# Optimization experiments

Measured on AMD Instinct MI355X. Metric: run time of the kernel, lower is better.

## Reference

```python
import jax, jax.numpy as jnp
import numpy as np

B, N, D, H, NCB, TOPK = 4, 2048, 256, 2048, 256, 16
DP = D // 4
SCALE = float(np.sqrt(DP))
THRESH = 0.7
EPS = 1e-8


def setup_inputs() -> dict:
    key = jax.random.key(0)
    ks = jax.random.split(key, 12)
    g = lambda i, shape, s=1.0: jax.random.normal(ks[i], shape, jnp.float32) * s
    return {
        "agent_states": g(0, (B, N, D)),
        "agent_actions": g(1, (B, N, D)),
        "episodic_mem": g(2, (B, N, H)),
        "Wq": g(3, (D, DP), 0.05), "bq": jnp.zeros((DP,), jnp.float32),
        "Wk": g(4, (D, DP), 0.05), "bk": jnp.zeros((DP,), jnp.float32),
        "log_temp": jnp.asarray(0.0, jnp.float32),
        "Wc": g(5, (D, DP), 0.05), "bc": jnp.zeros((DP,), jnp.float32),
        "temp_coal": jnp.asarray(10.0, jnp.float32),
        "W_to_hdc": g(6, (D, H), 0.05), "b_to_hdc": jnp.zeros((H,), jnp.float32),
        "W_from_hdc": g(7, (H, D), 0.02), "b_from_hdc": jnp.zeros((D,), jnp.float32),
        "agent_keys": jnp.sign(g(8, (N, H))),
        "position_codes": jnp.sign(g(9, (NCB, H))),
        "step": 3,
    }


def _cosine(a, b):
    # torch F.cosine_similarity semantics, dim=-1, eps=1e-8
    na = jnp.maximum(jnp.linalg.norm(a, axis=-1), EPS)
    nb = jnp.maximum(jnp.linalg.norm(b, axis=-1), EPS)
    return jnp.sum(a * b, axis=-1) / (na * nb)


def _to_hdc_ste(x):
    soft = jnp.tanh(x * 3.0)
    hard = jnp.sign(x)
    hard = jnp.where(hard == 0, jnp.ones_like(hard), hard)
    return soft + jax.lax.stop_gradient(hard - soft)


def reference(agent_states, agent_actions, episodic_mem, Wq, bq, Wk, bk,
              log_temp, Wc, bc, temp_coal, W_to_hdc, b_to_hdc,
              W_from_hdc, b_from_hdc, agent_keys, position_codes, step):
    # ---- DynamicGraph.compute_graph: top-k dynamic attention adjacency ----
    Q = agent_actions @ Wq + bq                      # (B,N,DP)
    K = agent_actions @ Wk + bk                      # (B,N,DP)
    temp = jnp.clip(jnp.exp(log_temp), 0.1, 10.0)
    scores = jnp.einsum('bnd,bmd->bnm', Q, K) / (SCALE * temp)   # (B,N,N)
    _, topk_idx = jax.lax.top_k(scores, TOPK)                     # (B,N,k)
    bI = jnp.arange(B)[:, None, None]
    nI = jnp.arange(N)[None, :, None]
    mask = jnp.zeros_like(scores).at[bI, nI, topk_idx].set(1.0)   # scatter, like torch scatter_
    scores = scores * mask + (1.0 - mask) * -1e9
    adjacency = jax.nn.softmax(scores, axis=-1)
    # message passing over dynamic graph
    incoming = jnp.einsum('bnm,bmd->bnd', adjacency, agent_states)

    # ---- AgentCombination: sigmoid-normalized coalition mixing ----
    proj = agent_actions @ Wc + bc                   # (B,N,DP)
    pn = proj / jnp.maximum(jnp.linalg.norm(proj, axis=-1, keepdims=True), 1e-12)
    sim = jnp.einsum('bnd,bmd->bnm', pn, pn)
    cw = jax.nn.sigmoid((sim - THRESH) * temp_coal)
    cw = cw / (jnp.sum(cw, axis=-1, keepdims=True) + EPS)
    combined = jnp.einsum('bnm,bmd->bnd', cw, incoming)
    mixed = 0.8 * incoming + 0.2 * combined          # (B,N,D)

    # ---- HDCMemory: bind / write / read with STE ----
    q = _to_hdc_ste(mixed @ W_to_hdc + b_to_hdc)     # (B,N,H) bipolar via STE
    pq = q * agent_keys[None]                        # bind with agent key
    mem = jax.lax.stop_gradient(episodic_mem)        # memory read is detached in original
    pos_code = position_codes[step % NCB]            # (H,)
    new_mem = 0.95 * mem + 0.05 * (q * pos_code)     # write: bind + decay bundle
    strength = jax.nn.sigmoid(_cosine(new_mem, pq))[..., None]   # read similarity
    recall = (new_mem @ W_from_hdc + b_from_hdc) * strength      # (B,N,D)
    return mixed + recall
```

## Files before the change

kernel.cpp:

```cpp
#include <hip/hip_runtime.h>
#include <math.h>

#define BATCH 4
#define NN 2048
#define DD 256
#define HH 2048
#define DP 64
#define KTOP 16

typedef float f32x4 __attribute__((ext_vector_type(4)));
typedef short short8 __attribute__((ext_vector_type(8)));
typedef short short4v __attribute__((ext_vector_type(4)));

__device__ __forceinline__ short f2bf(float x) {
    union { float f; unsigned u; } v; v.f = x;
    unsigned r = v.u + 0x7FFFu + ((v.u >> 16) & 1u);
    return (short)(r >> 16);
}
__device__ __forceinline__ float bf2f(short s) {
    union { unsigned u; float f; } v; v.u = ((unsigned)(unsigned short)s) << 16;
    return v.f;
}

__global__ __launch_bounds__(256) void head_kernel(
    const float* __restrict__ act,
    const float* __restrict__ Wq, const float* __restrict__ bq,
    const float* __restrict__ Wk, const float* __restrict__ bk,
    const float* __restrict__ Wc, const float* __restrict__ bc,
    const float* __restrict__ W2h, const float* __restrict__ Wfh,
    float* __restrict__ Qo, float* __restrict__ Ko, short* __restrict__ Pno,
    short* __restrict__ W2hT_hi, short* __restrict__ W2hT_lo,
    short* __restrict__ WfhT_hi, short* __restrict__ WfhT_lo)
{
    __shared__ float smem[16 * 256];

    if (blockIdx.x < 512) {
        float (*rowbuf)[256] = (float(*)[256])smem;
        const int row0 = blockIdx.x * 16;
        const int t = threadIdx.x;
        const int wave = t >> 6, lane = t & 63;
        const float* src = act + (size_t)row0 * DD;
        for (int i = t; i < 16 * DD; i += 256) rowbuf[i >> 8][i & 255] = src[i];
        __syncthreads();

        float q[4], k[4], c[4];
        #pragma unroll
        for (int r = 0; r < 4; ++r) { q[r] = bq[lane]; k[r] = bk[lane]; c[r] = bc[lane]; }

        for (int d = 0; d < DD; ++d) {
            float wq = Wq[d * DP + lane];
            float wk = Wk[d * DP + lane];
            float wc = Wc[d * DP + lane];
            #pragma unroll
            for (int r = 0; r < 4; ++r) {
                float av = rowbuf[wave * 4 + r][d];
                q[r] = fmaf(av, wq, q[r]);
                k[r] = fmaf(av, wk, k[r]);
                c[r] = fmaf(av, wc, c[r]);
            }
        }
        #pragma unroll
        for (int r = 0; r < 4; ++r) {
            float ss = c[r] * c[r];
            #pragma unroll
            for (int off = 32; off; off >>= 1) ss += __shfl_xor(ss, off);
            float nrm = fmaxf(sqrtf(ss), 1e-12f);
            size_t o = (size_t)(row0 + wave * 4 + r) * DP + lane;
            Qo[o] = q[r];
            Ko[o] = k[r];
            Pno[o] = f2bf(c[r] / nrm);
        }
    } else {
        float (*tile)[33] = (float(*)[33])smem;
        int b = blockIdx.x - 512;
        const float* src; short *dhi, *dlo; int R, C, r0, c0;
        if (b < 512) {
            src = W2h; dhi = W2hT_hi; dlo = W2hT_lo; R = 256; C = 2048;
            r0 = (b >> 6) * 32; c0 = (b & 63) * 32;
        } else {
            b -= 512;
            src = Wfh; dhi = WfhT_hi; dlo = WfhT_lo; R = 2048; C = 256;
            r0 = (b >> 3) * 32; c0 = (b & 7) * 32;
        }
        int tx = threadIdx.x & 31, ty = threadIdx.x >> 5;
        #pragma unroll
        for (int i = 0; i < 4; ++i)
            tile[ty + 8 * i][tx] = src[(size_t)(r0 + ty + 8 * i) * C + c0 + tx];
        __syncthreads();
        #pragma unroll
        for (int i = 0; i < 4; ++i) {
            float v = tile[tx][ty + 8 * i];
            short hi = f2bf(v);
            size_t o = (size_t)(c0 + ty + 8 * i) * R + r0 + tx;
            dhi[o] = hi;
            dlo[o] = f2bf(v - bf2f(hi));
        }
    }
}

__global__ __launch_bounds__(512, 4) void attn_fused_kernel(
    const float* __restrict__ Q, const float* __restrict__ K,
    const float* __restrict__ log_temp,
    const float* __restrict__ states, float* __restrict__ incoming)
{
    const int t = threadIdx.x;
    const int w = t >> 6, l = t & 63;
    const int row = blockIdx.x * 8 + w;
    const int b = row >> 11;

    __shared__ float Ksh[128][68];

    const float temp = fminf(fmaxf(expf(log_temp[0]), 0.1f), 10.0f);
    const float scale = 1.0f / (8.0f * temp);

    const float* Kb = K + (size_t)b * NN * DP;
    const float4* qr4 = (const float4*)(Q + (size_t)row * DP);

    float sc[32];

    for (int ch = 0; ch < 16; ++ch) {
        __syncthreads();
        {
            int r = t >> 2, seg = t & 3;
            const float4* src = (const float4*)(Kb + (size_t)(ch * 128 + r) * DP + seg * 16);
            float4* dst = (float4*)&Ksh[r][seg * 16];
            dst[0] = src[0]; dst[1] = src[1]; dst[2] = src[2]; dst[3] = src[3];
        }
        __syncthreads();
        float a0 = 0.f, a1 = 0.f;
        const float4* k0 = (const float4*)&Ksh[l][0];
        const float4* k1 = (const float4*)&Ksh[64 + l][0];
        #pragma unroll
        for (int h = 0; h < 2; ++h) {
            float4 q[8];
            #pragma unroll
            for (int i = 0; i < 8; ++i) q[i] = qr4[h * 8 + i];
            #pragma unroll
            for (int i = 0; i < 8; ++i) {
                float4 kv0 = k0[h * 8 + i];
                float4 kv1 = k1[h * 8 + i];
                a0 = fmaf(kv0.x, q[i].x, fmaf(kv0.y, q[i].y, fmaf(kv0.z, q[i].z, fmaf(kv0.w, q[i].w, a0))));
                a1 = fmaf(kv1.x, q[i].x, fmaf(kv1.y, q[i].y, fmaf(kv1.z, q[i].z, fmaf(kv1.w, q[i].w, a1))));
            }
        }
        sc[ch * 2]     = a0 * scale;
        sc[ch * 2 + 1] = a1 * scale;
    }

    float wv = 0.f; int wm = 0;
    for (int it = 0; it < KTOP; ++it) {
        float bv = sc[0]; int bs = 0;
        #pragma unroll
        for (int i = 1; i < 32; ++i) {
            bool g = sc[i] > bv;
            bv = g ? sc[i] : bv;
            bs = g ? i : bs;
        }
        int bm = (bs >> 1) * 128 + (bs & 1) * 64 + l;
        #pragma unroll
        for (int off = 1; off < 64; off <<= 1) {
            float ov = __shfl_xor(bv, off);
            int   om = __shfl_xor(bm, off);
            bool take = (ov > bv) || (ov == bv && om < bm);
            bv = take ? ov : bv;
            bm = take ? om : bm;
        }
        if (l == it) { wv = bv; wm = bm; }
        if ((bm & 63) == l) {
            int s = ((bm >> 7) << 1) | ((bm >> 6) & 1);
            #pragma unroll
            for (int i = 0; i < 32; ++i) if (s == i) sc[i] = -3.0e38f;
        }
    }

    float mx = __shfl(wv, 0);
    float e = (l < KTOP) ? expf(wv - mx) : 0.f;
    float Z = e;
    #pragma unroll
    for (int off = 1; off < 64; off <<= 1) Z += __shfl_xor(Z, off);
    float wnorm = e / Z;

    const float* Sb = states + (size_t)b * NN * DD;
    f32x4 acc = (f32x4){0.f, 0.f, 0.f, 0.f};
    #pragma unroll
    for (int kk = 0; kk < KTOP; ++kk) {
        float wk = __shfl(wnorm, kk);
        int   ik = __shfl(wm, kk);
        const float4 v = *(const float4*)(Sb + (size_t)ik * DD + l * 4);
        acc[0] = fmaf(wk, v.x, acc[0]);
        acc[1] = fmaf(wk, v.y, acc[1]);
        acc[2] = fmaf(wk, v.z, acc[2]);
        acc[3] = fmaf(wk, v.w, acc[3]);
    }
    *(float4*)(incoming + (size_t)row * DD + l * 4) = *(float4*)&acc;
}

__global__ __launch_bounds__(256) void coal_kernel(
    const short* __restrict__ pnb_g, const float* __restrict__ incoming,
    const float* __restrict__ temp_coal, float* __restrict__ mixed)
{
    const int b  = blockIdx.x >> 7;
    const int rem = blockIdx.x & 127;
    const int n0 = (rem >> 1) * 32;
    const int dh = rem & 1;
    const int t = threadIdx.x;
    const int w = t >> 6;
    const int l = t & 63;

    __shared__ alignas(16) short pnA[32][72];
    __shared__ alignas(16) short pnB[64][72];
    __shared__ alignas(16) short cwt[32][72];
    __shared__ alignas(16) short incT[128][72];
    __shared__ float rowsum[32];

    const size_t bbase = (size_t)b * NN;

    {
        int r = t >> 3, k8 = (t & 7) * 8;
        *(short8*)&pnA[r][k8] = *(const short8*)(pnb_g + (bbase + n0 + r) * DP + k8);
    }
    if (t < 32) rowsum[t] = 0.0f;

    const float tc = temp_coal[0];

    f32x4 acc[2][2];
    #pragma unroll
    for (int i = 0; i < 2; ++i)
        #pragma unroll
        for (int j = 0; j < 2; ++j)
            acc[i][j] = (f32x4){0.f, 0.f, 0.f, 0.f};

    const int lrow = l & 15;
    const int lk   = (l >> 4) * 8;

    for (int ch = 0; ch < 32; ++ch) {
        const int m0 = ch * 64;
        __syncthreads();

        {
            int r = t >> 2, kq = (t & 3) * 16;
            const short* src = pnb_g + (bbase + m0 + r) * DP + kq;
            *(short8*)&pnB[r][kq]     = *(const short8*)src;
            *(short8*)&pnB[r][kq + 8] = *(const short8*)(src + 8);
        }
        {
            int d4 = t & 31;
            int mg = t >> 5;
            const float* incb = incoming + (bbase + m0) * DD + dh * 128 + d4 * 4;
            #pragma unroll
            for (int i = 0; i < 8; ++i) {
                int m = mg * 8 + i;
                float4 v = *(const float4*)(incb + (size_t)m * DD);
                int db = d4 * 4;
                incT[db + 0][m] = f2bf(v.x);
                incT[db + 1][m] = f2bf(v.y);
                incT[db + 2][m] = f2bf(v.z);
                incT[db + 3][m] = f2bf(v.w);
            }
        }
        __syncthreads();

        f32x4 sacc[2];
        sacc[0] = (f32x4){0.f, 0.f, 0.f, 0.f};
        sacc[1] = (f32x4){0.f, 0.f, 0.f, 0.f};
        #pragma unroll
        for (int ks = 0; ks < 2; ++ks) {
            short8 bfr = *(const short8*)&pnB[w * 16 + lrow][lk + ks * 32];
            short8 a0  = *(const short8*)&pnA[lrow][lk + ks * 32];
            short8 a1  = *(const short8*)&pnA[16 + lrow][lk + ks * 32];
            sacc[0] = __builtin_amdgcn_mfma_f32_16x16x32_bf16(a0, bfr, sacc[0], 0, 0, 0);
            sacc[1] = __builtin_amdgcn_mfma_f32_16x16x32_bf16(a1, bfr, sacc[1], 0, 0, 0);
        }
        #pragma unroll
        for (int rt = 0; rt < 2; ++rt) {
            #pragma unroll
            for (int j = 0; j < 4; ++j) {
                int rr = rt * 16 + (l >> 4) * 4 + j;
                int cc = w * 16 + lrow;
                float cv = 1.0f / (1.0f + expf(-(sacc[rt][j] - 0.7f) * tc));
                cwt[rr][cc] = f2bf(cv);
            }
        }
        __syncthreads();

        {
            int r = t >> 3, c8 = (t & 7) * 8;
            short8 cv = *(const short8*)&cwt[r][c8];
            float p = 0.f;
            #pragma unroll
            for (int j = 0; j < 8; ++j) p += bf2f(cv[j]);
            p += __shfl_xor(p, 1);
            p += __shfl_xor(p, 2);
            p += __shfl_xor(p, 4);
            if ((t & 7) == 0) rowsum[r] += p;
        }

        #pragma unroll
        for (int ks = 0; ks < 2; ++ks) {
            short8 a0 = *(const short8*)&cwt[lrow][lk + ks * 32];
            short8 a1 = *(const short8*)&cwt[16 + lrow][lk + ks * 32];
            #pragma unroll
            for (int ct = 0; ct < 2; ++ct) {
                short8 bfr = *(const short8*)&incT[w * 32 + ct * 16 + lrow][lk + ks * 32];
                acc[0][ct] = __builtin_amdgcn_mfma_f32_16x16x32_bf16(a0, bfr, acc[0][ct], 0, 0, 0);
                acc[1][ct] = __builtin_amdgcn_mfma_f32_16x16x32_bf16(a1, bfr, acc[1][ct], 0, 0, 0);
            }
        }
    }
    __syncthreads();

    #pragma unroll
    for (int rt = 0; rt < 2; ++rt) {
        #pragma unroll
        for (int ct = 0; ct < 2; ++ct) {
            #pragma unroll
            for (int j = 0; j < 4; ++j) {
                int rr = rt * 16 + (l >> 4) * 4 + j;
                int cc = w * 32 + ct * 16 + lrow;
                float inv = 1.0f / (rowsum[rr] + 1e-8f);
                float comb = acc[rt][ct][j] * inv;
                size_t gi = (bbase + n0 + rr) * DD + dh * 128 + cc;
                mixed[gi] = 0.8f * incoming[gi] + 0.2f * comb;
            }
        }
    }
}

__global__ __launch_bounds__(256) void hdcA_kernel(
    const float* __restrict__ mixed,
    const short* __restrict__ W2hT_hi, const short* __restrict__ W2hT_lo,
    const float* __restrict__ b2h,
    unsigned short* __restrict__ qbits)
{
    const int rb = blockIdx.x >> 3;
    const int hs = blockIdx.x & 7;
    const int row0 = rb * 32;
    const int hbase = hs * 256;
    const int t = threadIdx.x;
    const int w = t >> 6, l = t & 63;
    const int lr = l & 15, lg = l >> 4;

    __shared__ short Ahi[32][264], Alo[32][264];
    __shared__ short Whi[64][136], Wlo[64][136];

    #pragma unroll
    for (int i = 0; i < 8; ++i) {
        int idx = t + i * 256;
        int r = idx >> 6, c = (idx & 63) * 4;
        float4 v = *(const float4*)(mixed + (size_t)(row0 + r) * DD + c);
        short4v hi4, lo4;
        hi4[0] = f2bf(v.x); lo4[0] = f2bf(v.x - bf2f(hi4[0]));
        hi4[1] = f2bf(v.y); lo4[1] = f2bf(v.y - bf2f(hi4[1]));
        hi4[2] = f2bf(v.z); lo4[2] = f2bf(v.z - bf2f(hi4[2]));
        hi4[3] = f2bf(v.w); lo4[3] = f2bf(v.w - bf2f(hi4[3]));
        *(short4v*)&Ahi[r][c] = hi4;
        *(short4v*)&Alo[r][c] = lo4;
    }

    for (int ch = 0; ch < 4; ++ch) {
        const int h0 = hbase + ch * 64;
        f32x4 zac[2];
        zac[0] = (f32x4){0.f, 0.f, 0.f, 0.f};
        zac[1] = (f32x4){0.f, 0.f, 0.f, 0.f};
        #pragma unroll
        for (int ks = 0; ks < 2; ++ks) {
            const int k0 = ks * 128;
            __syncthreads();
            {
                int r = t >> 2, cb = (t & 3) * 32;
                const short* sh = W2hT_hi + (size_t)(h0 + r) * DD + k0 + cb;
                const short* sl = W2hT_lo + (size_t)(h0 + r) * DD + k0 + cb;
                #pragma unroll
                for (int j = 0; j < 4; ++j) {
                    *(short8*)&Whi[r][cb + j * 8] = *(const short8*)(sh + j * 8);
                    *(short8*)&Wlo[r][cb + j * 8] = *(const short8*)(sl + j * 8);
                }
            }
            __syncthreads();
            #pragma unroll
            for (int kt = 0; kt < 4; ++kt) {
                int kk = k0 + kt * 32 + lg * 8;
                int kw = kt * 32 + lg * 8;
                short8 bhi = *(const short8*)&Whi[w * 16 + lr][kw];
                short8 blo = *(const short8*)&Wlo[w * 16 + lr][kw];
                #pragma unroll
                for (int mt = 0; mt < 2; ++mt) {
                    short8 ahi = *(const short8*)&Ahi[mt * 16 + lr][kk];
                    short8 alo = *(const short8*)&Alo[mt * 16 + lr][kk];
                    zac[mt] = __builtin_amdgcn_mfma_f32_16x16x32_bf16(ahi, bhi, zac[mt], 0, 0, 0);
                    zac[mt] = __builtin_amdgcn_mfma_f32_16x16x32_bf16(ahi, blo, zac[mt], 0, 0, 0);
                    zac[mt] = __builtin_amdgcn_mfma_f32_16x16x32_bf16(alo, bhi, zac[mt], 0, 0, 0);
                }
            }
        }
        const float bv = b2h[h0 + w * 16 + lr];
        #pragma unroll
        for (int mt = 0; mt < 2; ++mt) {
            #pragma unroll
            for (int j = 0; j < 4; ++j) {
                float z = zac[mt][j] + bv;
                unsigned long long bal = __ballot(z >= 0.0f);
                if (lr == 0)
                    qbits[(size_t)(row0 + mt * 16 + lg * 4 + j) * 128 + (h0 >> 4) + w] =
                        (unsigned short)((bal >> (lg * 16)) & 0xFFFFull);
            }
        }
    }
}

__global__ __launch_bounds__(512) void hdcB_kernel(
    const float* __restrict__ mem, const unsigned short* __restrict__ qbits,
    const float* __restrict__ pos_codes, const int* __restrict__ step,
    const short* __restrict__ WfhT_hi,
    const float* __restrict__ bfh, const float* __restrict__ keys,
    const float* __restrict__ mixed, float* __restrict__ out)
{
    const int mb = blockIdx.x >> 1, nb = blockIdx.x & 1;
    const int row0 = mb * 32, d0 = nb * 128;
    const int t = threadIdx.x;
    const int w = t >> 6, l = t & 63;
    const int wm = w >> 2, wn = w & 3;
    const int lr = l & 15, lg = l >> 4;

    __shared__ short Ahi[32][72], Alo[32][72];
    __shared__ short Bhi[128][72];
    __shared__ float sred[32][2];
    __shared__ float strenL[32];

    int st = ((step[0] % 256) + 256) % 256;
    const float* pos = pos_codes + (size_t)st * HH;

    f32x4 acc[2];
    acc[0] = (f32x4){0.f, 0.f, 0.f, 0.f};
    acc[1] = (f32x4){0.f, 0.f, 0.f, 0.f};
    float pnum = 0.f, pns = 0.f;

    const int ar = t >> 4;
    const int ah = (t & 15) * 4;
    const int arow = row0 + ar;
    const size_t memb = (size_t)arow * HH;
    const size_t keyb = (size_t)(arow & (NN - 1)) * HH;

    for (int kc = 0; kc < 32; ++kc) {
        const int h0 = kc * 64;
        __syncthreads();
        {
            float4 mv = *(const float4*)(mem + memb + h0 + ah);
            float4 kv = *(const float4*)(keys + keyb + h0 + ah);
            float4 pv = *(const float4*)(pos + h0 + ah);
            unsigned bits = (unsigned)qbits[(size_t)arow * 128 + ((h0 + ah) >> 4)] >> (ah & 15);
            float mvs[4] = { mv.x, mv.y, mv.z, mv.w };
            float kvs[4] = { kv.x, kv.y, kv.z, kv.w };
            float pvs[4] = { pv.x, pv.y, pv.z, pv.w };
            short4v hi4, lo4;
            #pragma unroll
            for (int j = 0; j < 4; ++j) {
                float q = ((bits >> j) & 1u) ? 1.0f : -1.0f;
                float nmv = fmaf(0.05f * q, pvs[j], 0.95f * mvs[j]);
                pnum = fmaf(nmv, q * kvs[j], pnum);
                pns  = fmaf(nmv, nmv, pns);
                hi4[j] = f2bf(nmv);
                lo4[j] = f2bf(nmv - bf2f(hi4[j]));
            }
            *(short4v*)&Ahi[ar][ah] = hi4;
            *(short4v*)&Alo[ar][ah] = lo4;
        }
        {
            int r = t >> 2, hb = (t & 3) * 16;
            const short* sh = WfhT_hi + (size_t)(d0 + r) * HH + h0 + hb;
            *(short8*)&Bhi[r][hb]     = *(const short8*)sh;
            *(short8*)&Bhi[r][hb + 8] = *(const short8*)(sh + 8);
        }
        __syncthreads();
        #pragma unroll
        for (int kt = 0; kt < 2; ++kt) {
            const int kk = kt * 32 + lg * 8;
            short8 ahi = *(const short8*)&Ahi[wm * 16 + lr][kk];
            short8 alo = *(const short8*)&Alo[wm * 16 + lr][kk];
            #pragma unroll
            for (int nt = 0; nt < 2; ++nt) {
                short8 bhi = *(const short8*)&Bhi[wn * 32 + nt * 16 + lr][kk];
                acc[nt] = __builtin_amdgcn_mfma_f32_16x16x32_bf16(ahi, bhi, acc[nt], 0, 0, 0);
                acc[nt] = __builtin_amdgcn_mfma_f32_16x16x32_bf16(alo, bhi, acc[nt], 0, 0, 0);
            }
        }
    }

    #pragma unroll
    for (int off = 1; off < 16; off <<= 1) {
        pnum += __shfl_xor(pnum, off);
        pns  += __shfl_xor(pns, off);
    }
    if ((t & 15) == 0) { sred[ar][0] = pnum; sred[ar][1] = pns; }
    __syncthreads();
    if (t < 32) {
        float cosv = sred[t][0] / (fmaxf(sqrtf(sred[t][1]), 1e-8f) * sqrtf(2048.0f));
        strenL[t] = 1.0f / (1.0f + expf(-cosv));
    }
    __syncthreads();

    #pragma unroll
    for (int nt = 0; nt < 2; ++nt) {
        #pragma unroll
        for (int j = 0; j < 4; ++j) {
            int rloc = wm * 16 + lg * 4 + j;
            int col = d0 + wn * 32 + nt * 16 + lr;
            size_t gi = (size_t)(row0 + rloc) * DD + col;
            out[gi] = mixed[gi] + (acc[nt][j] + bfh[col]) * strenL[rloc];
        }
    }
}

extern "C" void kernel_launch(void* const* d_in, const int* in_sizes, int n_in,
                              void* d_out, int out_size, void* d_ws, size_t ws_size,
                              hipStream_t stream) {
    const float* states    = (const float*)d_in[0];
    const float* actions   = (const float*)d_in[1];
    const float* mem       = (const float*)d_in[2];
    const float* Wq        = (const float*)d_in[3];
    const float* bq        = (const float*)d_in[4];
    const float* Wk        = (const float*)d_in[5];
    const float* bk        = (const float*)d_in[6];
    const float* log_temp  = (const float*)d_in[7];
    const float* Wc        = (const float*)d_in[8];
    const float* bc        = (const float*)d_in[9];
    const float* temp_coal = (const float*)d_in[10];
    const float* W2h       = (const float*)d_in[11];
    const float* b2h       = (const float*)d_in[12];
    const float* Wfh       = (const float*)d_in[13];
    const float* bfh       = (const float*)d_in[14];
    const float* keys      = (const float*)d_in[15];
    const float* pos_codes = (const float*)d_in[16];
    const int*   step      = (const int*)d_in[17];
    float* out = (float*)d_out;

    float* ws = (float*)d_ws;
    float* mixed    = ws;
    short* W2hT_hi  = (short*)(mixed + 2097152);
    short* W2hT_lo  = W2hT_hi + 524288;
    short* WfhT_hi  = W2hT_lo + 524288;
    short* WfhT_lo  = WfhT_hi + 524288;
    unsigned short* qbits = (unsigned short*)(WfhT_lo + 524288);
    float* Q        = (float*)(qbits + 1048576);
    float* K        = Q + 524288;
    float* incoming = K + 524288;
    short* pn_bf    = (short*)(incoming + 2097152);

    head_kernel<<<1536, 256, 0, stream>>>(actions, Wq, bq, Wk, bk, Wc, bc, W2h, Wfh,
                                          Q, K, pn_bf, W2hT_hi, W2hT_lo, WfhT_hi, WfhT_lo);
    attn_fused_kernel<<<BATCH * NN / 8, 512, 0, stream>>>(Q, K, log_temp, states, incoming);
    coal_kernel<<<BATCH * (NN / 32) * 2, 256, 0, stream>>>(pn_bf, incoming, temp_coal, mixed);
    hdcA_kernel<<<(BATCH * NN / 32) * 8, 256, 0, stream>>>(mixed, W2hT_hi, W2hT_lo, b2h, qbits);
    hdcB_kernel<<<(BATCH * NN / 32) * 2, 512, 0, stream>>>(mem, qbits, pos_codes, step,
                                                           WfhT_hi, bfh, keys, mixed, out);
}
```

Baseline: 336.4 us.

## Compute attention scores with split-bf16 MFMA instead of scalar FP32 FMAs

The head kernel now splits Q and K into three bf16 parts (hi, mid, lo), and the attention kernel computes QK^T scores with six bf16 MFMA products that approximate FP32 accuracy. The scores go into a shared-memory buffer, and each wave then reads back its row for the existing top-k selection. This replaces the scalar FMA loop and its staging of K tiles in LDS. It adds extra MFMA work and Q/K traffic, uses a 64KB shared buffer that limits occupancy, and small rounding differences could change top-k ties. The qbits buffer now aliases Qh, which is reused after the attention kernel finishes.

New measurement: 356.2 us. +5.9%, slower.

```diff
diff --git a/kernel.cpp b/kernel.cpp
--- a/kernel.cpp
+++ b/kernel.cpp
@@ -28,7 +28,9 @@
     const float* __restrict__ Wk, const float* __restrict__ bk,
     const float* __restrict__ Wc, const float* __restrict__ bc,
     const float* __restrict__ W2h, const float* __restrict__ Wfh,
-    float* __restrict__ Qo, float* __restrict__ Ko, short* __restrict__ Pno,
+    short* __restrict__ Qh, short* __restrict__ Qm, short* __restrict__ Ql,
+    short* __restrict__ Kh, short* __restrict__ Km, short* __restrict__ Kl,
+    short* __restrict__ Pno,
     short* __restrict__ W2hT_hi, short* __restrict__ W2hT_lo,
     short* __restrict__ WfhT_hi, short* __restrict__ WfhT_lo)
 {
@@ -66,8 +68,12 @@
             for (int off = 32; off; off >>= 1) ss += __shfl_xor(ss, off);
             float nrm = fmaxf(sqrtf(ss), 1e-12f);
             size_t o = (size_t)(row0 + wave * 4 + r) * DP + lane;
-            Qo[o] = q[r];
-            Ko[o] = k[r];
+            short h1 = f2bf(q[r]); float rs = q[r] - bf2f(h1);
+            short m1 = f2bf(rs);   rs -= bf2f(m1);
+            Qh[o] = h1; Qm[o] = m1; Ql[o] = f2bf(rs);
+            h1 = f2bf(k[r]); rs = k[r] - bf2f(h1);
+            m1 = f2bf(rs);   rs -= bf2f(m1);
+            Kh[o] = h1; Km[o] = m1; Kl[o] = f2bf(rs);
             Pno[o] = f2bf(c[r] / nrm);
         }
     } else {
@@ -98,54 +104,66 @@
     }
 }
 
-__global__ __launch_bounds__(512, 4) void attn_fused_kernel(
-    const float* __restrict__ Q, const float* __restrict__ K,
+__global__ __launch_bounds__(512) void attn_fused_kernel(
+    const short* __restrict__ Qh, const short* __restrict__ Qm, const short* __restrict__ Ql,
+    const short* __restrict__ Kh, const short* __restrict__ Km, const short* __restrict__ Kl,
     const float* __restrict__ log_temp,
     const float* __restrict__ states, float* __restrict__ incoming)
 {
     const int t = threadIdx.x;
     const int w = t >> 6, l = t & 63;
-    const int row = blockIdx.x * 8 + w;
-    const int b = row >> 11;
-
-    __shared__ float Ksh[128][68];
+    const int lr = l & 15, lg = l >> 4;
+    const int row0 = blockIdx.x * 8;
+    const int b = row0 >> 11;
+    const int row = row0 + w;
+
+    __shared__ float scbuf[8][2048];
 
     const float temp = fminf(fmaxf(expf(log_temp[0]), 0.1f), 10.0f);
     const float scale = 1.0f / (8.0f * temp);
 
-    const float* Kb = K + (size_t)b * NN * DP;
-    const float4* qr4 = (const float4*)(Q + (size_t)row * DP);
+    const size_t qoff = (size_t)(row0 + (lr & 7)) * DP;
+    short8 ah[2], am[2], al[2];
+    #pragma unroll
+    for (int ks = 0; ks < 2; ++ks) {
+        const size_t qa = qoff + ks * 32 + lg * 8;
+        ah[ks] = *(const short8*)(Qh + qa);
+        am[ks] = *(const short8*)(Qm + qa);
+        al[ks] = *(const short8*)(Ql + qa);
+    }
+
+    const size_t kbase = (size_t)b * NN * DP;
+
+    for (int tt = 0; tt < 16; ++tt) {
+        const int m0 = (tt * 8 + w) * 16;
+        const size_t koff = kbase + (size_t)(m0 + lr) * DP;
+        f32x4 accA = (f32x4){0.f, 0.f, 0.f, 0.f};
+        f32x4 accB = (f32x4){0.f, 0.f, 0.f, 0.f};
+        #pragma unroll
+        for (int ks = 0; ks < 2; ++ks) {
+            const size_t ka = koff + ks * 32 + lg * 8;
+            short8 bh = *(const short8*)(Kh + ka);
+            short8 bm = *(const short8*)(Km + ka);
+            short8 bl = *(const short8*)(Kl + ka);
+            accA = __builtin_amdgcn_mfma_f32_16x16x32_bf16(ah[ks], bh, accA, 0, 0, 0);
+            accB = __builtin_amdgcn_mfma_f32_16x16x32_bf16(ah[ks], bm, accB, 0, 0, 0);
+            accA = __builtin_amdgcn_mfma_f32_16x16x32_bf16(am[ks], bh, accA, 0, 0, 0);
+            accB = __builtin_amdgcn_mfma_f32_16x16x32_bf16(ah[ks], bl, accB, 0, 0, 0);
+            accA = __builtin_amdgcn_mfma_f32_16x16x32_bf16(al[ks], bh, accA, 0, 0, 0);
+            accB = __builtin_amdgcn_mfma_f32_16x16x32_bf16(am[ks], bm, accB, 0, 0, 0);
+        }
+        if (lg < 2) {
+            #pragma unroll
+            for (int j = 0; j < 4; ++j)
+                scbuf[lg * 4 + j][m0 + lr] = (accA[j] + accB[j]) * scale;
+        }
+    }
+    __syncthreads();
 
     float sc[32];
-
-    for (int ch = 0; ch < 16; ++ch) {
-        __syncthreads();
-        {
-            int r = t >> 2, seg = t & 3;
-            const float4* src = (const float4*)(Kb + (size_t)(ch * 128 + r) * DP + seg * 16);
-            float4* dst = (float4*)&Ksh[r][seg * 16];
-            dst[0] = src[0]; dst[1] = src[1]; dst[2] = src[2]; dst[3] = src[3];
-        }
-        __syncthreads();
-        float a0 = 0.f, a1 = 0.f;
-        const float4* k0 = (const float4*)&Ksh[l][0];
-        const float4* k1 = (const float4*)&Ksh[64 + l][0];
-        #pragma unroll
-        for (int h = 0; h < 2; ++h) {
-            float4 q[8];
-            #pragma unroll
-            for (int i = 0; i < 8; ++i) q[i] = qr4[h * 8 + i];
-            #pragma unroll
-            for (int i = 0; i < 8; ++i) {
-                float4 kv0 = k0[h * 8 + i];
-                float4 kv1 = k1[h * 8 + i];
-                a0 = fmaf(kv0.x, q[i].x, fmaf(kv0.y, q[i].y, fmaf(kv0.z, q[i].z, fmaf(kv0.w, q[i].w, a0))));
-                a1 = fmaf(kv1.x, q[i].x, fmaf(kv1.y, q[i].y, fmaf(kv1.z, q[i].z, fmaf(kv1.w, q[i].w, a1))));
-            }
-        }
-        sc[ch * 2]     = a0 * scale;
-        sc[ch * 2 + 1] = a1 * scale;
-    }
+    #pragma unroll
+    for (int s = 0; s < 32; ++s)
+        sc[s] = scbuf[w][(s >> 1) * 128 + (s & 1) * 64 + l];
 
     float wv = 0.f; int wm = 0;
     for (int it = 0; it < KTOP; ++it) {
@@ -540,15 +558,21 @@
     short* W2hT_lo  = W2hT_hi + 524288;
     short* WfhT_hi  = W2hT_lo + 524288;
     short* WfhT_lo  = WfhT_hi + 524288;
-    unsigned short* qbits = (unsigned short*)(WfhT_lo + 524288);
-    float* Q        = (float*)(qbits + 1048576);
-    float* K        = Q + 524288;
-    float* incoming = K + 524288;
+    short* Qh       = WfhT_lo + 524288;
+    short* Qm       = Qh + 524288;
+    short* Ql       = Qm + 524288;
+    short* Kh       = Ql + 524288;
+    short* Km       = Kh + 524288;
+    short* Kl       = Km + 524288;
+    float* incoming = (float*)(Kl + 524288);
     short* pn_bf    = (short*)(incoming + 2097152);
+    unsigned short* qbits = (unsigned short*)Qh;
 
     head_kernel<<<1536, 256, 0, stream>>>(actions, Wq, bq, Wk, bk, Wc, bc, W2h, Wfh,
-                                          Q, K, pn_bf, W2hT_hi, W2hT_lo, WfhT_hi, WfhT_lo);
-    attn_fused_kernel<<<BATCH * NN / 8, 512, 0, stream>>>(Q, K, log_temp, states, incoming);
+                                          Qh, Qm, Ql, Kh, Km, Kl, pn_bf,
+                                          W2hT_hi, W2hT_lo, WfhT_hi, WfhT_lo);
+    attn_fused_kernel<<<BATCH * NN / 8, 512, 0, stream>>>(Qh, Qm, Ql, Kh, Km, Kl,
+                                                          log_temp, states, incoming);
     coal_kernel<<<BATCH * (NN / 32) * 2, 256, 0, stream>>>(pn_bf, incoming, temp_coal, mixed);
     hdcA_kernel<<<(BATCH * NN / 32) * 8, 256, 0, stream>>>(mixed, W2hT_hi, W2hT_lo, b2h, qbits);
     hdcB_kernel<<<(BATCH * NN / 32) * 2, 512, 0, stream>>>(mem, qbits, pos_codes, step,
```
